# Kernel tuning notes

Measured on AMD Instinct MI355X. Metric: run time of the kernel, lower is better.

## Reference

```python
import jax, jax.numpy as jnp
import numpy as np

B, T, I, H, A = 1024, 2048, 8, 256, 8
DT = 0.1
EPS = 1e-5

def _layernorm(x, g, b):
    m = jnp.mean(x, axis=-1, keepdims=True)
    v = jnp.mean(jnp.square(x - m), axis=-1, keepdims=True)
    return (x - m) * jax.lax.rsqrt(v + EPS) * g + b

def setup_inputs() -> dict:
    key = jax.random.key(0)
    ks = jax.random.split(key, 8)
    xav = float(np.sqrt(6.0 / (H + H)))  # xavier_uniform for rec_weights
    return {
        "x": jax.random.normal(ks[0], (B, T, I), dtype=jnp.float32),
        "W_in": jax.random.normal(ks[1], (I, H), dtype=jnp.float32) * (1.0 / np.sqrt(I)),
        "b_in": jnp.zeros((H,), dtype=jnp.float32),
        "tau_param": jnp.ones((H,), dtype=jnp.float32),
        "W_rec": jax.random.uniform(ks[2], (H, H), dtype=jnp.float32, minval=-xav, maxval=xav),
        "g1": jnp.ones((H,), dtype=jnp.float32),
        "beta1": jnp.zeros((H,), dtype=jnp.float32),
        "g2": jnp.ones((H,), dtype=jnp.float32),
        "beta2": jnp.zeros((H,), dtype=jnp.float32),
        "head_w": jax.random.normal(ks[3], (H, A), dtype=jnp.float32) * (1.0 / np.sqrt(H)),
        "head_b": jnp.zeros((A,), dtype=jnp.float32),
    }

def reference(x, W_in, b_in, tau_param, W_rec, g1, beta1, g2, beta2, head_w, head_b):
    tau = jax.nn.softplus(tau_param)  # [H], broadcast over batch
    # Precompute input projection for all timesteps in one GEMM: [B,T,H]
    u = jnp.einsum("bti,ih->bth", x, W_in) + b_in
    u_t = jnp.swapaxes(u, 0, 1)  # [T,B,H] for scan

    def step(h, u_step):
        f = jnp.tanh(_layernorm(u_step + h @ W_rec, g1, beta1))
        h = jnp.clip(h + (-h / tau + f) * DT, -10.0, 10.0)
        return h, None

    h0 = jnp.zeros((x.shape[0], W_rec.shape[0]), dtype=x.dtype)
    h, _ = jax.lax.scan(step, h0, u_t)
    # per-appliance linear heads, fused into one matmul: [B, A]
    return _layernorm(h, g2, beta2) @ head_w + head_b
```

## Files before the change

### kernel.cpp

```cpp
#include <hip/hip_runtime.h>
#include <hip/hip_bf16.h>

#define T_ 2048
#define B_ 1024
#define H_ 256
#define I_ 8
#define A_ 8
#define DT_ 0.1f
#define EPS_ 1e-5f
#define LSTR 304
#define CH 32
#define RB 4

typedef __attribute__((ext_vector_type(8))) short bf16x8;
typedef __attribute__((ext_vector_type(4))) float f32x4;

#if __has_builtin(__builtin_amdgcn_cvt_pk_bf16_f32)
typedef __attribute__((ext_vector_type(2))) __bf16 bf16x2;
__device__ __forceinline__ int pk2bf(float a, float b) {
    bf16x2 r = __builtin_amdgcn_cvt_pk_bf16_f32(a, b);
    return __builtin_bit_cast(int, r);
}
#else
__device__ __forceinline__ short f2bf1(float f) {
    unsigned u = __builtin_bit_cast(unsigned, f);
    u += 0x7fffu + ((u >> 16) & 1u);
    return (short)(u >> 16);
}
__device__ __forceinline__ int pk2bf(float a, float b) {
    return (int)(unsigned short)f2bf1(a) | ((int)f2bf1(b) << 16);
}
#endif

__launch_bounds__(512, 2)
__global__ void liquid_kernel(const float* __restrict__ x,
                              const float* __restrict__ W_in,
                              const float* __restrict__ b_in,
                              const float* __restrict__ tau_param,
                              const float* __restrict__ W_rec,
                              const float* __restrict__ g1,
                              const float* __restrict__ beta1,
                              const float* __restrict__ g2,
                              const float* __restrict__ beta2,
                              const float* __restrict__ head_w,
                              const float* __restrict__ head_b,
                              float* __restrict__ out) {
    __shared__ short  h_lds[RB * LSTR];
    __shared__ short  xstage[2][CH][RB][8];
    __shared__ alignas(16) int zero16[4];
    __shared__ alignas(16) float2 redt[RB][10];
    __shared__ float  hw[H_ * A_];
    __shared__ float  outp[8][RB][A_];

    const int tid  = threadIdx.x;
    const int w    = tid >> 6;
    const int lane = tid & 63;
    const int quad = lane >> 4;
    const int l15  = lane & 15;
    const int row  = l15 & 3;
    const int cj   = l15 >> 2;
    const int mtj  = cj >> 1;
    const int rbs  = (cj & 1) * 2;
    const int r0   = blockIdx.x * RB;

    for (int i = tid; i < RB * LSTR; i += 512) h_lds[i] = 0;
    if (tid < 4) zero16[tid] = 0;

    f32x4 pbin0, pbin1;
    float p_g1s[2], p_b1s[2], p_decay[2];
#pragma unroll
    for (int r = 0; r < 4; ++r) {
        pbin0[r] = b_in[w * 32 + quad * 4 + r];
        pbin1[r] = b_in[w * 32 + 16 + quad * 4 + r];
    }
#pragma unroll
    for (int s = 0; s < 2; ++s) {
        int c = w * 32 + mtj * 16 + quad * 4 + rbs + s;
        p_g1s[s] = g1[c] * 2.885390082f;
        p_b1s[s] = beta1[c] * 2.885390082f;
        float tp = tau_param[c];
        float sp = (tp > 20.f) ? tp : log1pf(expf(tp));
        p_decay[s] = 1.0f - DT_ / sp;
    }

    bf16x8 afrag[2][9];
#pragma unroll
    for (int mt = 0; mt < 2; ++mt) {
        int cA = w * 32 + mt * 16 + l15;
#pragma unroll
        for (int ks = 0; ks < 9; ++ks) {
            bf16x8 f;
#pragma unroll
            for (int j = 0; j < 8; ++j) {
                int kg = ks * 32 + quad * 8 + j;
                float v;
                if (kg < 256)      v = W_rec[kg * H_ + cA];
                else if (kg < 264) v = W_in[(kg - 256) * H_ + cA];
                else               v = 0.f;
                f[j] = (short)pk2bf(v, v);
            }
            afrag[mt][ks] = f;
        }
    }

    const int xrow = (tid >> 6) & 3, xf4 = tid & 63;
    const int xt = xf4 >> 1, xi0 = (xf4 & 1) * 4;
    const bool xldr = (tid < 256);
    const float* xrbase = x + (size_t)(r0 + xrow) * T_ * I_;
    float4 xr;

    if (xldr) {
        xr = ((const float4*)xrbase)[xf4];
        int2 pk = make_int2(pk2bf(xr.x, xr.y), pk2bf(xr.z, xr.w));
        *reinterpret_cast<int2*>(&xstage[0][xt][xrow][xi0]) = pk;
        xr = ((const float4*)(xrbase + (size_t)CH * I_))[xf4];
    }

    float hreg[2];
    hreg[0] = 0.f; hreg[1] = 0.f;

    const short* hrow = &h_lds[row * LSTR + quad * 8];
    const f32x4 zacc = {0.f, 0.f, 0.f, 0.f};

    for (int t = 0; t < T_; ++t) {
        const int tc  = t & (CH - 1);
        const int c   = t >> 5;
        const int buf = c & 1;

        __syncthreads();

        if (xldr && tc == 16) {
            int2 pk = make_int2(pk2bf(xr.x, xr.y), pk2bf(xr.z, xr.w));
            *reinterpret_cast<int2*>(&xstage[buf ^ 1][xt][xrow][xi0]) = pk;
        }
        if (xldr && tc == 18) {
            int cc = c + 2; if (cc > (T_ / CH) - 1) cc = (T_ / CH) - 1;
            xr = ((const float4*)(xrbase + (size_t)cc * CH * I_))[xf4];
        }

        const short* xb = (quad == 0) ? &xstage[buf][tc][row][0] : (const short*)zero16;
        f32x4 c0a = pbin0, c1a = pbin1, c0b = zacc, c1b = zacc;
#pragma unroll
        for (int ks = 0; ks < 4; ++ks) {
            bf16x8 bA = *reinterpret_cast<const bf16x8*>(hrow + ks * 32);
            bf16x8 bB = *reinterpret_cast<const bf16x8*>(hrow + (ks + 4) * 32);
            c0a = __builtin_amdgcn_mfma_f32_16x16x32_bf16(afrag[0][ks],     bA, c0a, 0, 0, 0);
            c1a = __builtin_amdgcn_mfma_f32_16x16x32_bf16(afrag[1][ks],     bA, c1a, 0, 0, 0);
            c0b = __builtin_amdgcn_mfma_f32_16x16x32_bf16(afrag[0][ks + 4], bB, c0b, 0, 0, 0);
            c1b = __builtin_amdgcn_mfma_f32_16x16x32_bf16(afrag[1][ks + 4], bB, c1b, 0, 0, 0);
        }
        {
            bf16x8 b8 = *reinterpret_cast<const bf16x8*>(xb);
            c0a = __builtin_amdgcn_mfma_f32_16x16x32_bf16(afrag[0][8], b8, c0a, 0, 0, 0);
            c1a = __builtin_amdgcn_mfma_f32_16x16x32_bf16(afrag[1][8], b8, c1a, 0, 0, 0);
        }
        f32x4 acc0 = c0a + c0b, acc1 = c1a + c1b;

        float S  = ((acc0[0] + acc0[1]) + (acc0[2] + acc0[3]))
                 + ((acc1[0] + acc1[1]) + (acc1[2] + acc1[3]));
        float SQ = fmaf(acc0[0], acc0[0], fmaf(acc0[1], acc0[1],
                   fmaf(acc0[2], acc0[2], acc0[3] * acc0[3])))
                 + fmaf(acc1[0], acc1[0], fmaf(acc1[1], acc1[1],
                   fmaf(acc1[2], acc1[2], acc1[3] * acc1[3])));
        S += __shfl_xor(S, 16, 64);  SQ += __shfl_xor(SQ, 16, 64);
        S += __shfl_xor(S, 32, 64);  SQ += __shfl_xor(SQ, 32, 64);
        if (lane < RB) redt[row][w] = make_float2(S, SQ);

        __syncthreads();

        const float4* rrow = reinterpret_cast<const float4*>(&redt[row][0]);
        float4 q0 = rrow[0], q1 = rrow[1], q2 = rrow[2], q3 = rrow[3];
        float St  = ((q0.x + q0.z) + (q1.x + q1.z)) + ((q2.x + q2.z) + (q3.x + q3.z));
        float SQt = ((q0.y + q0.w) + (q1.y + q1.w)) + ((q2.y + q2.w) + (q3.y + q3.w));
        const float mu   = St * (1.f / 256.f);
        const float var  = fmaf(SQt, 1.f / 256.f, -mu * mu);
        const float rstd = __builtin_amdgcn_rsqf(var + EPS_);
        const float nmr  = -mu * rstd;

        f32x4 vsrc = mtj ? acc1 : acc0;
#pragma unroll
        for (int s = 0; s < 2; ++s) {
            float v  = vsrc[rbs + s];
            float tt = fmaf(v, rstd, nmr);
            float z2 = fmaf(tt, p_g1s[s], p_b1s[s]);
            float e  = __builtin_amdgcn_exp2f(z2);
            float rc = __builtin_amdgcn_rcpf(e + 1.f);
            float fd = fmaf(rc, -2.f * DT_, DT_);
            float h  = fmaf(hreg[s], p_decay[s], fd);
            hreg[s]  = __builtin_amdgcn_fmed3f(h, -10.f, 10.f);
        }
        *reinterpret_cast<int*>(&h_lds[row * LSTR + w * 32 + mtj * 16 + quad * 4 + rbs])
            = pk2bf(hreg[0], hreg[1]);
    }

    for (int i = tid; i < H_ * A_; i += 512) hw[i] = head_w[i];
    __syncthreads();

    float S2  = hreg[0] + hreg[1];
    float SQ2 = fmaf(hreg[0], hreg[0], hreg[1] * hreg[1]);
    S2 += __shfl_xor(S2, 4, 64);   SQ2 += __shfl_xor(SQ2, 4, 64);
    S2 += __shfl_xor(S2, 8, 64);   SQ2 += __shfl_xor(SQ2, 8, 64);
    S2 += __shfl_xor(S2, 16, 64);  SQ2 += __shfl_xor(SQ2, 16, 64);
    S2 += __shfl_xor(S2, 32, 64);  SQ2 += __shfl_xor(SQ2, 32, 64);
    if (lane < RB) redt[row][w] = make_float2(S2, SQ2);
    __syncthreads();
    const float4* rrow = reinterpret_cast<const float4*>(&redt[row][0]);
    float4 q0 = rrow[0], q1 = rrow[1], q2 = rrow[2], q3 = rrow[3];
    float St  = ((q0.x + q0.z) + (q1.x + q1.z)) + ((q2.x + q2.z) + (q3.x + q3.z));
    float SQt = ((q0.y + q0.w) + (q1.y + q1.w)) + ((q2.y + q2.w) + (q3.y + q3.w));
    const float mu   = St * (1.f / 256.f);
    const float var  = fmaf(SQt, 1.f / 256.f, -mu * mu);
    const float rstd = __builtin_amdgcn_rsqf(var + EPS_);

    float pa[8];
#pragma unroll
    for (int a = 0; a < 8; ++a) pa[a] = 0.f;
#pragma unroll
    for (int s = 0; s < 2; ++s) {
        int cc = w * 32 + mtj * 16 + quad * 4 + rbs + s;
        float lnh = (hreg[s] - mu) * rstd * g2[cc] + beta2[cc];
        float4 w0 = *reinterpret_cast<const float4*>(&hw[cc * 8]);
        float4 w1 = *reinterpret_cast<const float4*>(&hw[cc * 8 + 4]);
        pa[0] += lnh * w0.x; pa[1] += lnh * w0.y; pa[2] += lnh * w0.z; pa[3] += lnh * w0.w;
        pa[4] += lnh * w1.x; pa[5] += lnh * w1.y; pa[6] += lnh * w1.z; pa[7] += lnh * w1.w;
    }
#pragma unroll
    for (int a = 0; a < 8; ++a) {
        pa[a] += __shfl_xor(pa[a], 4, 64);
        pa[a] += __shfl_xor(pa[a], 8, 64);
        pa[a] += __shfl_xor(pa[a], 16, 64);
        pa[a] += __shfl_xor(pa[a], 32, 64);
    }
    if (lane < RB) {
#pragma unroll
        for (int a = 0; a < 8; ++a) outp[w][row][a] = pa[a];
    }
    __syncthreads();
    if (tid < RB * A_) {
        int r = tid >> 3, a = tid & 7;
        float s = head_b[a];
#pragma unroll
        for (int ww = 0; ww < 8; ++ww) s += outp[ww][r][a];
        out[(size_t)(r0 + r) * A_ + a] = s;
    }
}

extern "C" void kernel_launch(void* const* d_in, const int* in_sizes, int n_in,
                              void* d_out, int out_size, void* d_ws, size_t ws_size,
                              hipStream_t stream) {
    const float* x         = (const float*)d_in[0];
    const float* W_in      = (const float*)d_in[1];
    const float* b_in      = (const float*)d_in[2];
    const float* tau_param = (const float*)d_in[3];
    const float* W_rec     = (const float*)d_in[4];
    const float* g1        = (const float*)d_in[5];
    const float* beta1     = (const float*)d_in[6];
    const float* g2        = (const float*)d_in[7];
    const float* beta2     = (const float*)d_in[8];
    const float* head_w    = (const float*)d_in[9];
    const float* head_b    = (const float*)d_in[10];
    float* out = (float*)d_out;

    liquid_kernel<<<256, 512, 0, stream>>>(x, W_in, b_in, tau_param, W_rec,
                                           g1, beta1, g2, beta2, head_w, head_b, out);
}
```

Before: 1.766 ms.

## Halve rows per block and widen per-wave column tiles to four MFMA tiles

```diff
diff --git a/kernel.cpp b/kernel.cpp
--- a/kernel.cpp
+++ b/kernel.cpp
@@ -10,7 +10,8 @@
 #define EPS_ 1e-5f
 #define LSTR 304
 #define CH 32
-#define RB 4
+#define RB 2
+#define NW 4
 
 typedef __attribute__((ext_vector_type(8))) short bf16x8;
 typedef __attribute__((ext_vector_type(4))) float f32x4;
@@ -32,7 +33,7 @@
 }
 #endif
 
-__launch_bounds__(512, 2)
+__launch_bounds__(256, 2)
 __global__ void liquid_kernel(const float* __restrict__ x,
                               const float* __restrict__ W_in,
                               const float* __restrict__ b_in,
@@ -48,34 +49,34 @@
     __shared__ short  h_lds[RB * LSTR];
     __shared__ short  xstage[2][CH][RB][8];
     __shared__ alignas(16) int zero16[4];
-    __shared__ alignas(16) float2 redt[RB][10];
+    __shared__ alignas(16) float2 redt[RB][6];
     __shared__ float  hw[H_ * A_];
-    __shared__ float  outp[8][RB][A_];
+    __shared__ float  outp[NW][RB][A_];
 
     const int tid  = threadIdx.x;
     const int w    = tid >> 6;
     const int lane = tid & 63;
     const int quad = lane >> 4;
     const int l15  = lane & 15;
-    const int row  = l15 & 3;
-    const int cj   = l15 >> 2;
+    const int row  = l15 & 1;
+    const int cj   = l15 >> 1;
     const int mtj  = cj >> 1;
     const int rbs  = (cj & 1) * 2;
     const int r0   = blockIdx.x * RB;
 
-    for (int i = tid; i < RB * LSTR; i += 512) h_lds[i] = 0;
+    for (int i = tid; i < RB * LSTR; i += 256) h_lds[i] = 0;
     if (tid < 4) zero16[tid] = 0;
 
-    f32x4 pbin0, pbin1;
+    f32x4 pbin[4];
     float p_g1s[2], p_b1s[2], p_decay[2];
 #pragma unroll
-    for (int r = 0; r < 4; ++r) {
-        pbin0[r] = b_in[w * 32 + quad * 4 + r];
-        pbin1[r] = b_in[w * 32 + 16 + quad * 4 + r];
-    }
+    for (int mt = 0; mt < 4; ++mt)
+#pragma unroll
+        for (int r = 0; r < 4; ++r)
+            pbin[mt][r] = b_in[w * 64 + mt * 16 + quad * 4 + r];
 #pragma unroll
     for (int s = 0; s < 2; ++s) {
-        int c = w * 32 + mtj * 16 + quad * 4 + rbs + s;
+        int c = w * 64 + mtj * 16 + quad * 4 + rbs + s;
         p_g1s[s] = g1[c] * 2.885390082f;
         p_b1s[s] = beta1[c] * 2.885390082f;
         float tp = tau_param[c];
@@ -83,10 +84,10 @@
         p_decay[s] = 1.0f - DT_ / sp;
     }
 
-    bf16x8 afrag[2][9];
-#pragma unroll
-    for (int mt = 0; mt < 2; ++mt) {
-        int cA = w * 32 + mt * 16 + l15;
+    bf16x8 afrag[4][9];
+#pragma unroll
+    for (int mt = 0; mt < 4; ++mt) {
+        int cA = w * 64 + mt * 16 + l15;
 #pragma unroll
         for (int ks = 0; ks < 9; ++ks) {
             bf16x8 f;
@@ -103,9 +104,9 @@
         }
     }
 
-    const int xrow = (tid >> 6) & 3, xf4 = tid & 63;
+    const int xrow = (tid >> 6) & 1, xf4 = tid & 63;
     const int xt = xf4 >> 1, xi0 = (xf4 & 1) * 4;
-    const bool xldr = (tid < 256);
+    const bool xldr = (tid < 128);
     const float* xrbase = x + (size_t)(r0 + xrow) * T_ * I_;
     float4 xr;
 
@@ -139,29 +140,42 @@
         }
 
         const short* xb = (quad == 0) ? &xstage[buf][tc][row][0] : (const short*)zero16;
-        f32x4 c0a = pbin0, c1a = pbin1, c0b = zacc, c1b = zacc;
+        f32x4 ca0 = pbin[0], ca1 = pbin[1], ca2 = pbin[2], ca3 = pbin[3];
+        f32x4 cb0 = zacc, cb1 = zacc, cb2 = zacc, cb3 = zacc;
 #pragma unroll
         for (int ks = 0; ks < 4; ++ks) {
             bf16x8 bA = *reinterpret_cast<const bf16x8*>(hrow + ks * 32);
             bf16x8 bB = *reinterpret_cast<const bf16x8*>(hrow + (ks + 4) * 32);
-            c0a = __builtin_amdgcn_mfma_f32_16x16x32_bf16(afrag[0][ks],     bA, c0a, 0, 0, 0);
-            c1a = __builtin_amdgcn_mfma_f32_16x16x32_bf16(afrag[1][ks],     bA, c1a, 0, 0, 0);
-            c0b = __builtin_amdgcn_mfma_f32_16x16x32_bf16(afrag[0][ks + 4], bB, c0b, 0, 0, 0);
-            c1b = __builtin_amdgcn_mfma_f32_16x16x32_bf16(afrag[1][ks + 4], bB, c1b, 0, 0, 0);
+            ca0 = __builtin_amdgcn_mfma_f32_16x16x32_bf16(afrag[0][ks],     bA, ca0, 0, 0, 0);
+            ca1 = __builtin_amdgcn_mfma_f32_16x16x32_bf16(afrag[1][ks],     bA, ca1, 0, 0, 0);
+            ca2 = __builtin_amdgcn_mfma_f32_16x16x32_bf16(afrag[2][ks],     bA, ca2, 0, 0, 0);
+            ca3 = __builtin_amdgcn_mfma_f32_16x16x32_bf16(afrag[3][ks],     bA, ca3, 0, 0, 0);
+            cb0 = __builtin_amdgcn_mfma_f32_16x16x32_bf16(afrag[0][ks + 4], bB, cb0, 0, 0, 0);
+            cb1 = __builtin_amdgcn_mfma_f32_16x16x32_bf16(afrag[1][ks + 4], bB, cb1, 0, 0, 0);
+            cb2 = __builtin_amdgcn_mfma_f32_16x16x32_bf16(afrag[2][ks + 4], bB, cb2, 0, 0, 0);
+            cb3 = __builtin_amdgcn_mfma_f32_16x16x32_bf16(afrag[3][ks + 4], bB, cb3, 0, 0, 0);
         }
         {
             bf16x8 b8 = *reinterpret_cast<const bf16x8*>(xb);
-            c0a = __builtin_amdgcn_mfma_f32_16x16x32_bf16(afrag[0][8], b8, c0a, 0, 0, 0);
-            c1a = __builtin_amdgcn_mfma_f32_16x16x32_bf16(afrag[1][8], b8, c1a, 0, 0, 0);
-        }
-        f32x4 acc0 = c0a + c0b, acc1 = c1a + c1b;
-
-        float S  = ((acc0[0] + acc0[1]) + (acc0[2] + acc0[3]))
-                 + ((acc1[0] + acc1[1]) + (acc1[2] + acc1[3]));
-        float SQ = fmaf(acc0[0], acc0[0], fmaf(acc0[1], acc0[1],
-                   fmaf(acc0[2], acc0[2], acc0[3] * acc0[3])))
-                 + fmaf(acc1[0], acc1[0], fmaf(acc1[1], acc1[1],
-                   fmaf(acc1[2], acc1[2], acc1[3] * acc1[3])));
+            ca0 = __builtin_amdgcn_mfma_f32_16x16x32_bf16(afrag[0][8], b8, ca0, 0, 0, 0);
+            ca1 = __builtin_amdgcn_mfma_f32_16x16x32_bf16(afrag[1][8], b8, ca1, 0, 0, 0);
+            ca2 = __builtin_amdgcn_mfma_f32_16x16x32_bf16(afrag[2][8], b8, ca2, 0, 0, 0);
+            ca3 = __builtin_amdgcn_mfma_f32_16x16x32_bf16(afrag[3][8], b8, ca3, 0, 0, 0);
+        }
+        f32x4 acc0 = ca0 + cb0, acc1 = ca1 + cb1, acc2 = ca2 + cb2, acc3 = ca3 + cb3;
+
+        float S  = (((acc0[0] + acc0[1]) + (acc0[2] + acc0[3]))
+                 +  ((acc1[0] + acc1[1]) + (acc1[2] + acc1[3])))
+                 + (((acc2[0] + acc2[1]) + (acc2[2] + acc2[3]))
+                 +  ((acc3[0] + acc3[1]) + (acc3[2] + acc3[3])));
+        float SQ = (fmaf(acc0[0], acc0[0], fmaf(acc0[1], acc0[1],
+                    fmaf(acc0[2], acc0[2], acc0[3] * acc0[3])))
+                 +  fmaf(acc1[0], acc1[0], fmaf(acc1[1], acc1[1],
+                    fmaf(acc1[2], acc1[2], acc1[3] * acc1[3]))))
+                 + (fmaf(acc2[0], acc2[0], fmaf(acc2[1], acc2[1],
+                    fmaf(acc2[2], acc2[2], acc2[3] * acc2[3])))
+                 +  fmaf(acc3[0], acc3[0], fmaf(acc3[1], acc3[1],
+                    fmaf(acc3[2], acc3[2], acc3[3] * acc3[3]))));
         S += __shfl_xor(S, 16, 64);  SQ += __shfl_xor(SQ, 16, 64);
         S += __shfl_xor(S, 32, 64);  SQ += __shfl_xor(SQ, 32, 64);
         if (lane < RB) redt[row][w] = make_float2(S, SQ);
@@ -169,15 +183,16 @@
         __syncthreads();
 
         const float4* rrow = reinterpret_cast<const float4*>(&redt[row][0]);
-        float4 q0 = rrow[0], q1 = rrow[1], q2 = rrow[2], q3 = rrow[3];
-        float St  = ((q0.x + q0.z) + (q1.x + q1.z)) + ((q2.x + q2.z) + (q3.x + q3.z));
-        float SQt = ((q0.y + q0.w) + (q1.y + q1.w)) + ((q2.y + q2.w) + (q3.y + q3.w));
+        float4 q0 = rrow[0], q1 = rrow[1];
+        float St  = (q0.x + q0.z) + (q1.x + q1.z);
+        float SQt = (q0.y + q0.w) + (q1.y + q1.w);
         const float mu   = St * (1.f / 256.f);
         const float var  = fmaf(SQt, 1.f / 256.f, -mu * mu);
         const float rstd = __builtin_amdgcn_rsqf(var + EPS_);
         const float nmr  = -mu * rstd;
 
-        f32x4 vsrc = mtj ? acc1 : acc0;
+        f32x4 vsrc = (mtj & 2) ? ((mtj & 1) ? acc3 : acc2)
+                               : ((mtj & 1) ? acc1 : acc0);
 #pragma unroll
         for (int s = 0; s < 2; ++s) {
             float v  = vsrc[rbs + s];
@@ -189,15 +204,16 @@
             float h  = fmaf(hreg[s], p_decay[s], fd);
             hreg[s]  = __builtin_amdgcn_fmed3f(h, -10.f, 10.f);
         }
-        *reinterpret_cast<int*>(&h_lds[row * LSTR + w * 32 + mtj * 16 + quad * 4 + rbs])
+        *reinterpret_cast<int*>(&h_lds[row * LSTR + w * 64 + mtj * 16 + quad * 4 + rbs])
             = pk2bf(hreg[0], hreg[1]);
     }
 
-    for (int i = tid; i < H_ * A_; i += 512) hw[i] = head_w[i];
+    for (int i = tid; i < H_ * A_; i += 256) hw[i] = head_w[i];
     __syncthreads();
 
     float S2  = hreg[0] + hreg[1];
     float SQ2 = fmaf(hreg[0], hreg[0], hreg[1] * hreg[1]);
+    S2 += __shfl_xor(S2, 2, 64);   SQ2 += __shfl_xor(SQ2, 2, 64);
     S2 += __shfl_xor(S2, 4, 64);   SQ2 += __shfl_xor(SQ2, 4, 64);
     S2 += __shfl_xor(S2, 8, 64);   SQ2 += __shfl_xor(SQ2, 8, 64);
     S2 += __shfl_xor(S2, 16, 64);  SQ2 += __shfl_xor(SQ2, 16, 64);
@@ -205,9 +221,9 @@
     if (lane < RB) redt[row][w] = make_float2(S2, SQ2);
     __syncthreads();
     const float4* rrow = reinterpret_cast<const float4*>(&redt[row][0]);
-    float4 q0 = rrow[0], q1 = rrow[1], q2 = rrow[2], q3 = rrow[3];
-    float St  = ((q0.x + q0.z) + (q1.x + q1.z)) + ((q2.x + q2.z) + (q3.x + q3.z));
-    float SQt = ((q0.y + q0.w) + (q1.y + q1.w)) + ((q2.y + q2.w) + (q3.y + q3.w));
+    float4 q0 = rrow[0], q1 = rrow[1];
+    float St  = (q0.x + q0.z) + (q1.x + q1.z);
+    float SQt = (q0.y + q0.w) + (q1.y + q1.w);
     const float mu   = St * (1.f / 256.f);
     const float var  = fmaf(SQt, 1.f / 256.f, -mu * mu);
     const float rstd = __builtin_amdgcn_rsqf(var + EPS_);
@@ -217,7 +233,7 @@
     for (int a = 0; a < 8; ++a) pa[a] = 0.f;
 #pragma unroll
     for (int s = 0; s < 2; ++s) {
-        int cc = w * 32 + mtj * 16 + quad * 4 + rbs + s;
+        int cc = w * 64 + mtj * 16 + quad * 4 + rbs + s;
         float lnh = (hreg[s] - mu) * rstd * g2[cc] + beta2[cc];
         float4 w0 = *reinterpret_cast<const float4*>(&hw[cc * 8]);
         float4 w1 = *reinterpret_cast<const float4*>(&hw[cc * 8 + 4]);
@@ -226,6 +242,7 @@
     }
 #pragma unroll
     for (int a = 0; a < 8; ++a) {
+        pa[a] += __shfl_xor(pa[a], 2, 64);
         pa[a] += __shfl_xor(pa[a], 4, 64);
         pa[a] += __shfl_xor(pa[a], 8, 64);
         pa[a] += __shfl_xor(pa[a], 16, 64);
@@ -240,7 +257,7 @@
         int r = tid >> 3, a = tid & 7;
         float s = head_b[a];
 #pragma unroll
-        for (int ww = 0; ww < 8; ++ww) s += outp[ww][r][a];
+        for (int ww = 0; ww < NW; ++ww) s += outp[ww][r][a];
         out[(size_t)(r0 + r) * A_ + a] = s;
     }
 }
@@ -261,6 +278,6 @@
     const float* head_b    = (const float*)d_in[10];
     float* out = (float*)d_out;
 
-    liquid_kernel<<<256, 512, 0, stream>>>(x, W_in, b_in, tau_param, W_rec,
-                                           g1, beta1, g2, beta2, head_w, head_b, out);
-}
+    liquid_kernel<<<B_ / RB, 256, 0, stream>>>(x, W_in, b_in, tau_param, W_rec,
+                                               g1, beta1, g2, beta2, head_w, head_b, out);
+}
```

Measured after the change: 2.313 ms. 1.31x slower.

## Prefetch x fragment across barrier, use permlane swaps and lean barriers

Applied to the files above, without the earlier changes.

```diff
diff --git a/kernel.cpp b/kernel.cpp
--- a/kernel.cpp
+++ b/kernel.cpp
@@ -31,6 +31,21 @@
     return (int)(unsigned short)f2bf1(a) | ((int)f2bf1(b) << 16);
 }
 #endif
+
+__device__ __forceinline__ float foldswap16(float x) {
+    float a = x, b = x;
+    asm("v_permlane16_swap_b32 %0, %1" : "+v"(a), "+v"(b));
+    return a + b;
+}
+__device__ __forceinline__ float foldswap32(float x) {
+    float a = x, b = x;
+    asm("v_permlane32_swap_b32 %0, %1" : "+v"(a), "+v"(b));
+    return a + b;
+}
+
+__device__ __forceinline__ void bar_lgkm() {
+    asm volatile("s_waitcnt lgkmcnt(0)\n\ts_barrier" ::: "memory");
+}
 
 __launch_bounds__(512, 2)
 __global__ void liquid_kernel(const float* __restrict__ x,
@@ -47,7 +62,6 @@
                               float* __restrict__ out) {
     __shared__ short  h_lds[RB * LSTR];
     __shared__ short  xstage[2][CH][RB][8];
-    __shared__ alignas(16) int zero16[4];
     __shared__ alignas(16) float2 redt[RB][10];
     __shared__ float  hw[H_ * A_];
     __shared__ float  outp[8][RB][A_];
@@ -64,7 +78,6 @@
     const int r0   = blockIdx.x * RB;
 
     for (int i = tid; i < RB * LSTR; i += 512) h_lds[i] = 0;
-    if (tid < 4) zero16[tid] = 0;
 
     f32x4 pbin0, pbin1;
     float p_g1s[2], p_b1s[2], p_decay[2];
@@ -121,13 +134,19 @@
 
     const short* hrow = &h_lds[row * LSTR + quad * 8];
     const f32x4 zacc = {0.f, 0.f, 0.f, 0.f};
+    const bf16x8 zb = {0, 0, 0, 0, 0, 0, 0, 0};
+
+    __syncthreads();
+
+    bf16x8 xbr = zb;
+    if (quad == 0) xbr = *reinterpret_cast<const bf16x8*>(&xstage[0][0][row][0]);
 
     for (int t = 0; t < T_; ++t) {
         const int tc  = t & (CH - 1);
         const int c   = t >> 5;
         const int buf = c & 1;
 
-        __syncthreads();
+        bar_lgkm();
 
         if (xldr && tc == 16) {
             int2 pk = make_int2(pk2bf(xr.x, xr.y), pk2bf(xr.z, xr.w));
@@ -138,8 +157,9 @@
             xr = ((const float4*)(xrbase + (size_t)cc * CH * I_))[xf4];
         }
 
-        const short* xb = (quad == 0) ? &xstage[buf][tc][row][0] : (const short*)zero16;
         f32x4 c0a = pbin0, c1a = pbin1, c0b = zacc, c1b = zacc;
+        c0a = __builtin_amdgcn_mfma_f32_16x16x32_bf16(afrag[0][8], xbr, c0a, 0, 0, 0);
+        c1a = __builtin_amdgcn_mfma_f32_16x16x32_bf16(afrag[1][8], xbr, c1a, 0, 0, 0);
 #pragma unroll
         for (int ks = 0; ks < 4; ++ks) {
             bf16x8 bA = *reinterpret_cast<const bf16x8*>(hrow + ks * 32);
@@ -149,11 +169,6 @@
             c0b = __builtin_amdgcn_mfma_f32_16x16x32_bf16(afrag[0][ks + 4], bB, c0b, 0, 0, 0);
             c1b = __builtin_amdgcn_mfma_f32_16x16x32_bf16(afrag[1][ks + 4], bB, c1b, 0, 0, 0);
         }
-        {
-            bf16x8 b8 = *reinterpret_cast<const bf16x8*>(xb);
-            c0a = __builtin_amdgcn_mfma_f32_16x16x32_bf16(afrag[0][8], b8, c0a, 0, 0, 0);
-            c1a = __builtin_amdgcn_mfma_f32_16x16x32_bf16(afrag[1][8], b8, c1a, 0, 0, 0);
-        }
         f32x4 acc0 = c0a + c0b, acc1 = c1a + c1b;
 
         float S  = ((acc0[0] + acc0[1]) + (acc0[2] + acc0[3]))
@@ -162,11 +177,11 @@
                    fmaf(acc0[2], acc0[2], acc0[3] * acc0[3])))
                  + fmaf(acc1[0], acc1[0], fmaf(acc1[1], acc1[1],
                    fmaf(acc1[2], acc1[2], acc1[3] * acc1[3])));
-        S += __shfl_xor(S, 16, 64);  SQ += __shfl_xor(SQ, 16, 64);
-        S += __shfl_xor(S, 32, 64);  SQ += __shfl_xor(SQ, 32, 64);
+        S = foldswap16(S);  SQ = foldswap16(SQ);
+        S = foldswap32(S);  SQ = foldswap32(SQ);
         if (lane < RB) redt[row][w] = make_float2(S, SQ);
 
-        __syncthreads();
+        bar_lgkm();
 
         const float4* rrow = reinterpret_cast<const float4*>(&redt[row][0]);
         float4 q0 = rrow[0], q1 = rrow[1], q2 = rrow[2], q3 = rrow[3];
@@ -191,6 +206,14 @@
         }
         *reinterpret_cast<int*>(&h_lds[row * LSTR + w * 32 + mtj * 16 + quad * 4 + rbs])
             = pk2bf(hreg[0], hreg[1]);
+
+        {
+            const int tn  = (t + 1 < T_) ? t + 1 : t;
+            const int tcn = tn & (CH - 1), bufn = (tn >> 5) & 1;
+            xbr = zb;
+            if (quad == 0)
+                xbr = *reinterpret_cast<const bf16x8*>(&xstage[bufn][tcn][row][0]);
+        }
     }
 
     for (int i = tid; i < H_ * A_; i += 512) hw[i] = head_w[i];
```

Result: faster. 1.721 ms, median of 2 (-2.5%).
